# Kernel optimization log

Measured on AMD Instinct MI355X. Metric: run time of the kernel, lower is better.

The kernel has to match this reference:

```python
import jax, jax.numpy as jnp
import numpy as np

B, D = 32768, 256
M, K, V = 1024, 128, 128  # memory_units, key_size, memory_size


def setup_inputs() -> dict:
    key = jax.random.key(0)
    ks = jax.random.split(key, 13)
    g = lambda k, shape, fan: jax.random.normal(k, shape, jnp.float32) * (2.0 / sum(fan)) ** 0.5
    return {
        "x": jax.random.normal(ks[0], (B, D), jnp.float32),
        "Wk": g(ks[1], (D, K), (D, K)), "bk": jnp.zeros((K,), jnp.float32),
        "Wv": g(ks[2], (D, V), (D, V)), "bv": jnp.zeros((V,), jnp.float32),
        "Wq": g(ks[3], (D, K), (D, K)), "bq": jnp.zeros((K,), jnp.float32),
        "Wwr": g(ks[4], (M, M), (M, M)), "bwr": jnp.zeros((M,), jnp.float32),
        "Wrd": g(ks[5], (M, M), (M, M)), "brd": jnp.zeros((M,), jnp.float32),
        "key_memory": g(ks[6], (M, K), (M, K)),
        "value_memory": g(ks[7], (M, V), (M, V)),
    }


def reference(x, Wk, bk, Wv, bv, Wq, bq, Wwr, bwr, Wrd, brd, key_memory, value_memory):
    elu = jax.nn.elu
    key_vec = elu(x @ Wk + bk)      # [B, K]
    val_vec = elu(x @ Wv + bv)      # [B, V]
    qry_vec = elu(x @ Wq + bq)      # [B, K]

    # write attention: Dense(M, softmax) applied to [B, M] scores
    wscores = key_vec @ key_memory.T            # [B, M]
    write_w = jax.nn.softmax(wscores @ Wwr + bwr, axis=-1)  # [B, M]

    inv_b = jnp.float32(1.0 / B)
    # mean over batch of outer products == einsum / B (avoids [B, M, K] intermediate)
    key_mem_new = key_memory + jnp.einsum("bm,bk->mk", write_w, key_vec) * inv_b
    val_mem_new = value_memory + jnp.einsum("bm,bv->mv", write_w, val_vec) * inv_b

    # read uses the UPDATED memories (matches assign_add ordering in call)
    rscores = qry_vec @ key_mem_new.T            # [B, M]
    read_w = jax.nn.softmax(rscores @ Wrd + brd, axis=-1)
    read_vec = read_w @ val_mem_new              # [B, V]
    return read_vec
```

## Files before the change

kernel.cpp:

```cpp
#include <hip/hip_runtime.h>
#include <stdint.h>


typedef short bf16x8 __attribute__((ext_vector_type(8)));
typedef short s16x4  __attribute__((ext_vector_type(4)));
typedef float f32x4  __attribute__((ext_vector_type(4)));

#define MFMA(a, b, c) __builtin_amdgcn_mfma_f32_16x16x32_bf16((a), (b), (c), 0, 0, 0)

__device__ __forceinline__ short f2bf(float f) {
    union { float f; uint32_t u; } v; v.f = f;
    uint32_t r = (v.u + 0x7FFFu + ((v.u >> 16) & 1u)) >> 16;
    return (short)r;
}
__device__ __forceinline__ float bf2f(short h) {
    union { uint32_t u; float f; } v; v.u = ((uint32_t)(uint16_t)h) << 16;
    return v.f;
}
__device__ __forceinline__ uint32_t pack2(float a, float b) {
    return (uint32_t)(uint16_t)f2bf(a) | ((uint32_t)(uint16_t)f2bf(b) << 16);
}
__device__ __forceinline__ unsigned lds_addr(const void* p) {
    return (unsigned)(uintptr_t)(__attribute__((address_space(3))) const void*)p;
}
__device__ __forceinline__ s16x4 trrd(unsigned a) {
    s16x4 d;
    asm volatile("ds_read_b64_tr_b16 %0, %1" : "=v"(d) : "v"(a));
    return d;
}
__device__ __forceinline__ bf16x8 cat8(s16x4 lo, s16x4 hi) {
    bf16x8 r;
    r[0] = lo[0]; r[1] = lo[1]; r[2] = lo[2]; r[3] = lo[3];
    r[4] = hi[0]; r[5] = hi[1]; r[6] = hi[2]; r[7] = hi[3];
    return r;
}
#define GLDS(g, l) __builtin_amdgcn_global_load_lds(                          \
    (const __attribute__((address_space(1))) void*)(g),                       \
    (__attribute__((address_space(3))) void*)(l), 16, 0, 0)

__global__ void kw_kernel(const float* __restrict__ Wk, const float* __restrict__ Wv,
                          const float* __restrict__ Wq, short* __restrict__ wt) {
    const int c = blockIdx.x;
    const int d = threadIdx.x;
    const float* W = (c < 128) ? Wk : ((c < 256) ? Wv : Wq);
    wt[c * 256 + d] = f2bf(W[d * 128 + (c & 127)]);
}

__global__ __launch_bounds__(256) void proj_kernel(
    const float* __restrict__ x, const short* __restrict__ wt,
    const float* __restrict__ bk, const float* __restrict__ bv,
    const float* __restrict__ bq, short* __restrict__ kvq)
{
    const int tid = threadIdx.x;
    const int wave = tid >> 6, lane = tid & 63;
    const int l15 = lane & 15, lq = lane >> 4;
    const int r0 = blockIdx.x * 64;

    f32x4 acc[4][6];
    for (int i = 0; i < 4; ++i)
        for (int j = 0; j < 6; ++j) acc[i][j] = (f32x4){0.f, 0.f, 0.f, 0.f};

    for (int ks = 0; ks < 8; ++ks) {
        const int k0 = ks * 32 + lq * 8;
        bf16x8 a[4];
#pragma unroll
        for (int mf = 0; mf < 4; ++mf) {
            const float* xp = x + (long)(r0 + mf * 16 + l15) * 256 + k0;
            float4 u = *(const float4*)xp;
            float4 v = *(const float4*)(xp + 4);
            bf16x8 t;
            t[0] = f2bf(u.x); t[1] = f2bf(u.y); t[2] = f2bf(u.z); t[3] = f2bf(u.w);
            t[4] = f2bf(v.x); t[5] = f2bf(v.y); t[6] = f2bf(v.z); t[7] = f2bf(v.w);
            a[mf] = t;
        }
#pragma unroll
        for (int nf = 0; nf < 6; ++nf) {
            const int n = wave * 96 + nf * 16 + l15;
            bf16x8 b = *(const bf16x8*)(wt + n * 256 + k0);
#pragma unroll
            for (int mf = 0; mf < 4; ++mf) acc[mf][nf] = MFMA(a[mf], b, acc[mf][nf]);
        }
    }
#pragma unroll
    for (int nf = 0; nf < 6; ++nf) {
        const int col = wave * 96 + nf * 16 + l15;
        const float bias = (col < 128) ? bk[col] : ((col < 256) ? bv[col - 128] : bq[col - 256]);
#pragma unroll
        for (int mf = 0; mf < 4; ++mf) {
#pragma unroll
            for (int rr = 0; rr < 4; ++rr) {
                float v = acc[mf][nf][rr] + bias;
                v = (v > 0.f) ? v : (__expf(v) - 1.f);
                kvq[(long)(r0 + mf * 16 + lq * 4 + rr) * 384 + col] = f2bf(v);
            }
        }
    }
}

template <int COLS>
__global__ __launch_bounds__(256) void pgemm_kernel(
    const void* __restrict__ Agv, const void* __restrict__ Bgv,
    const int lda, const int ldb, const int rchunks, const int rstride,
    float* __restrict__ part)
{
    __shared__ __align__(16) short As[128][72];
    __shared__ __align__(16) short Bs[COLS][72];
    const int tid = threadIdx.x;
    const int wave = tid >> 6, lane = tid & 63;
    const int l15 = lane & 15, lq = lane >> 4;
    const int mt = blockIdx.x, rs = blockIdx.y;
    const long b0 = (long)rs * rstride;
    constexpr int NCF = COLS / 16;
    constexpr int CPT = COLS / 8;

    f32x4 acc[2][NCF];
    for (int s = 0; s < 2; ++s)
        for (int c = 0; c < NCF; ++c) acc[s][c] = (f32x4){0.f, 0.f, 0.f, 0.f};

    const int sr  = (tid & 31) * 2;
    const int am0 = (tid >> 5) * 16;
    const int bc0 = (tid >> 5) * CPT;

    for (int ch = 0; ch < rchunks; ++ch) {
        const long rb = b0 + (long)ch * 64;
        {
            const float* p0 = (const float*)Agv + (rb + sr) * lda + mt * 128 + am0;
            const float* p1 = p0 + lda;
#pragma unroll
            for (int j = 0; j < 16; ++j)
                *(uint32_t*)&As[am0 + j][sr] = pack2(p0[j], p1[j]);
        }
        {
            const float* p0 = (const float*)Bgv + (rb + sr) * ldb + bc0;
            const float* p1 = p0 + ldb;
#pragma unroll
            for (int j = 0; j < CPT; ++j)
                *(uint32_t*)&Bs[bc0 + j][sr] = pack2(p0[j], p1[j]);
        }
        __syncthreads();
#pragma unroll
        for (int ks = 0; ks < 2; ++ks) {
            bf16x8 a0 = *(const bf16x8*)&As[wave * 32 + l15][ks * 32 + lq * 8];
            bf16x8 a1 = *(const bf16x8*)&As[wave * 32 + 16 + l15][ks * 32 + lq * 8];
#pragma unroll
            for (int cf = 0; cf < NCF; ++cf) {
                bf16x8 b = *(const bf16x8*)&Bs[cf * 16 + l15][ks * 32 + lq * 8];
                acc[0][cf] = MFMA(a0, b, acc[0][cf]);
                acc[1][cf] = MFMA(a1, b, acc[1][cf]);
            }
        }
        __syncthreads();
    }
    float* pp = part + (long)rs * 1024 * COLS;
#pragma unroll
    for (int s = 0; s < 2; ++s)
#pragma unroll
        for (int cf = 0; cf < NCF; ++cf)
#pragma unroll
            for (int rr = 0; rr < 4; ++rr) {
                const int m = mt * 128 + wave * 32 + s * 16 + lq * 4 + rr;
                pp[(long)m * COLS + cf * 16 + l15] = acc[s][cf][rr];
            }
}

__global__ void finp_kernel(const float* __restrict__ part, short* __restrict__ pt) {
    const int i = blockIdx.x * 256 + threadIdx.x;
    float s = 0.f;
#pragma unroll
    for (int k = 0; k < 8; ++k) s += part[k * 131072 + i];
    pt[i] = f2bf(s);
}

__global__ __launch_bounds__(256) void eins_kernel(
    const short* __restrict__ w,
    const short* __restrict__ kvq,
    short* __restrict__ part)
{
    __shared__ __align__(16) short As[8192];
    __shared__ __align__(16) short Bs[8192];
    const int tid = threadIdx.x;
    const int wave = tid >> 6, lane = tid & 63;
    const int l15 = lane & 15, lq = lane >> 4;
    const int mt = blockIdx.x >> 1, ct = blockIdx.x & 1;
    const int ks = blockIdx.y;
    const long k0_blk = (long)ks * 1024;

    int aoff[4], boff[4];
    const short* ldsA[4];
    const short* ldsB[4];
#pragma unroll
    for (int q = 0; q < 4; ++q) {
        const int t = wave + q * 4;
        const int s = t * 8 + (lane >> 3);
        const int kl = (s & 15) * 4 + ((lane & 7) >> 1);
        const int m  = (s >> 4) * 16 + (lane & 1) * 8;
        aoff[q] = kl * 1024 + mt * 128 + m;
        boff[q] = kl * 384  + ct * 128 + m;
        ldsA[q] = &As[t * 512];
        ldsB[q] = &Bs[t * 512];
    }

    f32x4 acc[4][4];
    for (int i = 0; i < 4; ++i)
        for (int j = 0; j < 4; ++j) acc[i][j] = (f32x4){0.f, 0.f, 0.f, 0.f};

    const int wr = wave >> 1, wc = wave & 1;
    const unsigned trb  = lds_addr(As) + 2u * (l15 + lq * 64);
    const unsigned trbB = lds_addr(Bs) + 2u * (l15 + lq * 64);

    for (int ch = 0; ch < 16; ++ch) {
        const short* wa = w   + (k0_blk + ch * 64) * 1024;
        const short* kb = kvq + (k0_blk + ch * 64) * 384;
#pragma unroll
        for (int q = 0; q < 4; ++q) {
            GLDS(wa + aoff[q], ldsA[q]);
            GLDS(kb + boff[q], ldsB[q]);
        }
        __syncthreads();
#pragma unroll
        for (int kst = 0; kst < 2; ++kst) {
            s16x4 ah[4][2], bh[4][2];
#pragma unroll
            for (int f = 0; f < 4; ++f) {
#pragma unroll
                for (int h = 0; h < 2; ++h) {
                    ah[f][h] = trrd(trb  + 128u * ((wr * 4 + f) * 16 + kst * 8 + h * 4));
                    bh[f][h] = trrd(trbB + 128u * ((wc * 4 + f) * 16 + kst * 8 + h * 4));
                }
            }
            asm volatile("s_waitcnt lgkmcnt(0)" ::: "memory");
            __builtin_amdgcn_sched_barrier(0);
#pragma unroll
            for (int mf = 0; mf < 4; ++mf) {
                bf16x8 a = cat8(ah[mf][0], ah[mf][1]);
#pragma unroll
                for (int cf = 0; cf < 4; ++cf)
                    acc[mf][cf] = MFMA(a, cat8(bh[cf][0], bh[cf][1]), acc[mf][cf]);
            }
        }
        __syncthreads();
    }

    short* pp = part + ((long)ks * 1024 + mt * 128) * 256 + ct * 128;
#pragma unroll
    for (int mf = 0; mf < 4; ++mf)
#pragma unroll
        for (int cf = 0; cf < 4; ++cf)
#pragma unroll
            for (int rr = 0; rr < 4; ++rr) {
                const int m = wr * 64 + mf * 16 + lq * 4 + rr;
                const int c = wc * 64 + cf * 16 + l15;
                pp[(long)m * 256 + c] = f2bf(acc[mf][cf][rr]);
            }
}

__global__ void finmem_kernel(const short* __restrict__ part,
                              const float* __restrict__ km, const float* __restrict__ vm,
                              float* __restrict__ km_new, short* __restrict__ vmt) {
    const int m = blockIdx.x;
    const int c = threadIdx.x;
    float s = 0.f;
#pragma unroll
    for (int k = 0; k < 32; ++k) s += bf2f(part[k * 262144 + m * 256 + c]);
    s *= (1.0f / 32768.0f);
    if (c < 128) {
        km_new[m * 128 + c] = km[m * 128 + c] + s;
    } else {
        const int v = c - 128;
        vmt[v * 1024 + m] = f2bf(vm[m * 128 + v] + s);
    }
}

__global__ __launch_bounds__(1024, 4) void wexp_kernel(
    const short* __restrict__ kvq, const short* __restrict__ pt,
    const float* __restrict__ bias, short* __restrict__ wout)
{
    __shared__ __align__(16) char kt[16384];
    __shared__ float sred[16][64];
    __shared__ float invs[64];
    const int tid = threadIdx.x;
    const int wave = tid >> 6, lane = tid & 63;
    const int l15 = lane & 15, lq = lane >> 4;
    const int r0 = blockIdx.x * 64;
    const int n0 = wave * 64;

    {
        const int row = tid >> 4;
        const int colb = 16 * ((tid & 15) ^ (row & 7));
        GLDS((const char*)kvq + (long)(r0 + row) * 768 + colb, kt + tid * 16);
    }
    __syncthreads();

    f32x4 acc[4][4];
#pragma unroll
    for (int i = 0; i < 4; ++i)
#pragma unroll
        for (int j = 0; j < 4; ++j) acc[i][j] = (f32x4){0.f, 0.f, 0.f, 0.f};

#pragma unroll
    for (int ks = 0; ks < 4; ++ks) {
        bf16x8 a[4], b[4];
#pragma unroll
        for (int nf = 0; nf < 4; ++nf)
            a[nf] = *(const bf16x8*)(pt + (n0 + nf * 16 + l15) * 128 + ks * 32 + lq * 8);
#pragma unroll
        for (int bf = 0; bf < 4; ++bf) {
            const int r = bf * 16 + l15;
            const int cb = (ks * 64 + lq * 16) ^ ((r & 7) << 4);
            b[bf] = *(const bf16x8*)(kt + r * 256 + cb);
        }
#pragma unroll
        for (int nf = 0; nf < 4; ++nf)
#pragma unroll
            for (int bf = 0; bf < 4; ++bf)
                acc[nf][bf] = MFMA(a[nf], b[bf], acc[nf][bf]);
    }

    float s[4] = {0.f, 0.f, 0.f, 0.f};
#pragma unroll
    for (int nf = 0; nf < 4; ++nf) {
        float4 b4 = *(const float4*)(bias + n0 + nf * 16 + lq * 4);
#pragma unroll
        for (int bf = 0; bf < 4; ++bf) {
            f32x4 t = acc[nf][bf];
            t[0] = __expf(t[0] + b4.x);
            t[1] = __expf(t[1] + b4.y);
            t[2] = __expf(t[2] + b4.z);
            t[3] = __expf(t[3] + b4.w);
            acc[nf][bf] = t;
            s[bf] += (t[0] + t[1]) + (t[2] + t[3]);
        }
    }
#pragma unroll
    for (int bf = 0; bf < 4; ++bf) {
        s[bf] += __shfl_xor(s[bf], 16);
        s[bf] += __shfl_xor(s[bf], 32);
    }
    if (lq == 0) {
#pragma unroll
        for (int bf = 0; bf < 4; ++bf) sred[wave][bf * 16 + l15] = s[bf];
    }
    __syncthreads();
    if (tid < 64) {
        float t = 0.f;
#pragma unroll
        for (int wv = 0; wv < 16; ++wv) t += sred[wv][tid];
        invs[tid] = 1.f / t;
    }
    __syncthreads();

#pragma unroll
    for (int bf = 0; bf < 4; ++bf) {
        const float iv = invs[bf * 16 + l15];
        short* wp = wout + (long)(r0 + bf * 16 + l15) * 1024 + n0 + lq * 4;
#pragma unroll
        for (int nf = 0; nf < 4; ++nf) {
            f32x4 t = acc[nf][bf];
            *(uint2*)(wp + nf * 16) =
                (uint2){pack2(t[0] * iv, t[1] * iv), pack2(t[2] * iv, t[3] * iv)};
        }
    }
}

__global__ __launch_bounds__(1024, 4) void rexp_kernel(
    const short* __restrict__ kvq, const short* __restrict__ pt,
    const float* __restrict__ bias, const short* __restrict__ vmt,
    float* __restrict__ out)
{
    __shared__ __align__(16) char smem[132096];
    __shared__ float sred[16][64];
    __shared__ float invs[64];
    short* Elds = (short*)smem;
    char*  qt   = smem;
    const int tid = threadIdx.x;
    const int wave = tid >> 6, lane = tid & 63;
    const int l15 = lane & 15, lq = lane >> 4;
    const int r0 = blockIdx.x * 64;
    const int n0 = wave * 64;

    {
        const int row = tid >> 4;
        const int colb = 16 * ((tid & 15) ^ (row & 7));
        GLDS((const char*)kvq + (long)(r0 + row) * 768 + 512 + colb, qt + tid * 16);
    }
    __syncthreads();

    f32x4 acc[4][4];
#pragma unroll
    for (int i = 0; i < 4; ++i)
#pragma unroll
        for (int j = 0; j < 4; ++j) acc[i][j] = (f32x4){0.f, 0.f, 0.f, 0.f};

#pragma unroll
    for (int ks = 0; ks < 4; ++ks) {
        bf16x8 a[4], b[4];
#pragma unroll
        for (int nf = 0; nf < 4; ++nf)
            a[nf] = *(const bf16x8*)(pt + (n0 + nf * 16 + l15) * 128 + ks * 32 + lq * 8);
#pragma unroll
        for (int bf = 0; bf < 4; ++bf) {
            const int r = bf * 16 + l15;
            const int cb = (ks * 64 + lq * 16) ^ ((r & 7) << 4);
            b[bf] = *(const bf16x8*)(qt + r * 256 + cb);
        }
#pragma unroll
        for (int nf = 0; nf < 4; ++nf)
#pragma unroll
            for (int bf = 0; bf < 4; ++bf)
                acc[nf][bf] = MFMA(a[nf], b[bf], acc[nf][bf]);
    }

    float s[4] = {0.f, 0.f, 0.f, 0.f};
#pragma unroll
    for (int nf = 0; nf < 4; ++nf) {
        float4 b4 = *(const float4*)(bias + n0 + nf * 16 + lq * 4);
#pragma unroll
        for (int bf = 0; bf < 4; ++bf) {
            f32x4 t = acc[nf][bf];
            t[0] = __expf(t[0] + b4.x);
            t[1] = __expf(t[1] + b4.y);
            t[2] = __expf(t[2] + b4.z);
            t[3] = __expf(t[3] + b4.w);
            acc[nf][bf] = t;
            s[bf] += (t[0] + t[1]) + (t[2] + t[3]);
        }
    }
#pragma unroll
    for (int bf = 0; bf < 4; ++bf) {
        s[bf] += __shfl_xor(s[bf], 16);
        s[bf] += __shfl_xor(s[bf], 32);
    }
    if (lq == 0) {
#pragma unroll
        for (int bf = 0; bf < 4; ++bf) sred[wave][bf * 16 + l15] = s[bf];
    }
    __syncthreads();
    if (tid < 64) {
        float t = 0.f;
#pragma unroll
        for (int wv = 0; wv < 16; ++wv) t += sred[wv][tid];
        invs[tid] = 1.f / t;
    }
    __syncthreads();

#pragma unroll
    for (int bf = 0; bf < 4; ++bf) {
        const float iv = invs[bf * 16 + l15];
        short* ep = Elds + (bf * 16 + l15) * 1032 + n0 + lq * 4;
#pragma unroll
        for (int nf = 0; nf < 4; ++nf) {
            f32x4 t = acc[nf][bf];
            *(uint2*)(ep + nf * 16) =
                (uint2){pack2(t[0] * iv, t[1] * iv), pack2(t[2] * iv, t[3] * iv)};
        }
    }
    __syncthreads();

    const int vf = wave >> 1;
    const int bfp = (wave & 1) * 2;
    f32x4 pv0 = {0.f, 0.f, 0.f, 0.f}, pv1 = {0.f, 0.f, 0.f, 0.f};
    const short* er0 = Elds + (bfp * 16 + l15) * 1032 + lq * 8;
    const short* er1 = er0 + 16 * 1032;
    const short* vp  = vmt + (vf * 16 + l15) * 1024 + lq * 8;
#pragma unroll 8
    for (int ks = 0; ks < 32; ++ks) {
        bf16x8 bv = *(const bf16x8*)(vp + ks * 32);
        pv0 = MFMA(*(const bf16x8*)(er0 + ks * 32), bv, pv0);
        pv1 = MFMA(*(const bf16x8*)(er1 + ks * 32), bv, pv1);
    }
#pragma unroll
    for (int rr = 0; rr < 4; ++rr) {
        out[(long)(r0 + bfp * 16 + lq * 4 + rr) * 128 + vf * 16 + l15] = pv0[rr];
        out[(long)(r0 + (bfp + 1) * 16 + lq * 4 + rr) * 128 + vf * 16 + l15] = pv1[rr];
    }
}

extern "C" void kernel_launch(void* const* d_in, const int* in_sizes, int n_in,
                              void* d_out, int out_size, void* d_ws, size_t ws_size,
                              hipStream_t stream)
{
    const float* x   = (const float*)d_in[0];
    const float* Wk  = (const float*)d_in[1];
    const float* bk  = (const float*)d_in[2];
    const float* Wv  = (const float*)d_in[3];
    const float* bv  = (const float*)d_in[4];
    const float* Wq  = (const float*)d_in[5];
    const float* bq  = (const float*)d_in[6];
    const float* Wwr = (const float*)d_in[7];
    const float* bwr = (const float*)d_in[8];
    const float* Wrd = (const float*)d_in[9];
    const float* brd = (const float*)d_in[10];
    const float* km  = (const float*)d_in[11];
    const float* vm  = (const float*)d_in[12];
    float* out = (float*)d_out;

    char* ws = (char*)d_ws;
    short* kvq  = (short*)(ws + 0);
    short* w    = (short*)(ws + 25165824);
    float* part = (float*)(ws + 92274688);
    short* p1t  = (short*)(ws + 109051904);
    short* p2t  = (short*)(ws + 109314048);
    float* kmn  = (float*)(ws + 109576192);
    short* vmt  = (short*)(ws + 110100480);
    short* wt   = (short*)(ws + 110362624);
    if (ws_size < 110559232u) return;

    kw_kernel<<<384, 256, 0, stream>>>(Wk, Wv, Wq, wt);
    proj_kernel<<<512, 256, 0, stream>>>(x, wt, bk, bv, bq, kvq);
    pgemm_kernel<128><<<dim3(8, 8), 256, 0, stream>>>(Wwr, km, 1024, 128, 2, 128, part);
    finp_kernel<<<512, 256, 0, stream>>>(part, p1t);
    wexp_kernel<<<512, 1024, 0, stream>>>(kvq, p1t, bwr, w);
    eins_kernel<<<dim3(16, 32), 256, 0, stream>>>(w, kvq, (short*)part);
    finmem_kernel<<<1024, 256, 0, stream>>>((const short*)part, km, vm, kmn, vmt);
    pgemm_kernel<128><<<dim3(8, 8), 256, 0, stream>>>(Wrd, kmn, 1024, 128, 2, 128, part);
    finp_kernel<<<512, 256, 0, stream>>>(part, p2t);
    rexp_kernel<<<512, 1024, 0, stream>>>(kvq, p2t, brd, vmt, out);
}
```

Measured before the change: 203.9 us.

## Replace read softmax kernel with flash-attention style fused streaming kernel

The final read stage no longer materialises the full 64x1024 softmax row tile in LDS. Each wave now owns 16 rows and streams 64-column tiles of the score projection and value memory through small LDS buffers. It computes exp scores, packs them to bf16 and feeds them directly into a 16x16x16 MFMA against value memory, normalising once at the end. This cuts LDS footprint and block size (256 threads instead of 1024) and drops the block-wide reduction syncs, at the cost of per-tile barriers and global reloads of pt/vmt for every block.

```diff
diff --git a/kernel.cpp b/kernel.cpp
--- a/kernel.cpp
+++ b/kernel.cpp
@@ -7,6 +7,11 @@
 typedef float f32x4  __attribute__((ext_vector_type(4)));
 
 #define MFMA(a, b, c) __builtin_amdgcn_mfma_f32_16x16x32_bf16((a), (b), (c), 0, 0, 0)
+
+__device__ __forceinline__ f32x4 MFMA16(s16x4 a, s16x4 b, f32x4 c) {
+    asm("v_mfma_f32_16x16x16_bf16 %0, %1, %2, %0" : "+v"(c) : "v"(a), "v"(b));
+    return c;
+}
 
 __device__ __forceinline__ short f2bf(float f) {
     union { float f; uint32_t u; } v; v.f = f;
@@ -362,116 +367,109 @@
     }
 }
 
-__global__ __launch_bounds__(1024, 4) void rexp_kernel(
+__global__ __launch_bounds__(256, 4) void fatt_kernel(
     const short* __restrict__ kvq, const short* __restrict__ pt,
     const float* __restrict__ bias, const short* __restrict__ vmt,
     float* __restrict__ out)
 {
-    __shared__ __align__(16) char smem[132096];
-    __shared__ float sred[16][64];
-    __shared__ float invs[64];
-    short* Elds = (short*)smem;
-    char*  qt   = smem;
+    __shared__ __align__(16) char ptl[16384];
+    __shared__ __align__(16) char vtl[16384];
     const int tid = threadIdx.x;
     const int wave = tid >> 6, lane = tid & 63;
     const int l15 = lane & 15, lq = lane >> 4;
-    const int r0 = blockIdx.x * 64;
-    const int n0 = wave * 64;
-
-    {
-        const int row = tid >> 4;
-        const int colb = 16 * ((tid & 15) ^ (row & 7));
-        GLDS((const char*)kvq + (long)(r0 + row) * 768 + 512 + colb, qt + tid * 16);
-    }
-    __syncthreads();
-
-    f32x4 acc[4][4];
-#pragma unroll
-    for (int i = 0; i < 4; ++i)
-#pragma unroll
-        for (int j = 0; j < 4; ++j) acc[i][j] = (f32x4){0.f, 0.f, 0.f, 0.f};
-
-#pragma unroll
-    for (int ks = 0; ks < 4; ++ks) {
-        bf16x8 a[4], b[4];
-#pragma unroll
-        for (int nf = 0; nf < 4; ++nf)
-            a[nf] = *(const bf16x8*)(pt + (n0 + nf * 16 + l15) * 128 + ks * 32 + lq * 8);
-#pragma unroll
-        for (int bf = 0; bf < 4; ++bf) {
-            const int r = bf * 16 + l15;
-            const int cb = (ks * 64 + lq * 16) ^ ((r & 7) << 4);
-            b[bf] = *(const bf16x8*)(qt + r * 256 + cb);
-        }
-#pragma unroll
-        for (int nf = 0; nf < 4; ++nf)
-#pragma unroll
-            for (int bf = 0; bf < 4; ++bf)
-                acc[nf][bf] = MFMA(a[nf], b[bf], acc[nf][bf]);
-    }
-
-    float s[4] = {0.f, 0.f, 0.f, 0.f};
-#pragma unroll
-    for (int nf = 0; nf < 4; ++nf) {
-        float4 b4 = *(const float4*)(bias + n0 + nf * 16 + lq * 4);
-#pragma unroll
-        for (int bf = 0; bf < 4; ++bf) {
-            f32x4 t = acc[nf][bf];
+    const int r0 = blockIdx.x * 64 + wave * 16;
+
+    bf16x8 qf[4];
+#pragma unroll
+    for (int ks = 0; ks < 4; ++ks)
+        qf[ks] = *(const bf16x8*)(kvq + (long)(r0 + l15) * 384 + 256 + ks * 32 + lq * 8);
+
+    f32x4 o[8];
+#pragma unroll
+    for (int i = 0; i < 8; ++i) o[i] = (f32x4){0.f, 0.f, 0.f, 0.f};
+    float s = 0.f;
+
+    const char* ptb = (const char*)pt;
+    const char* vmb = (const char*)vmt;
+
+    int pn[4], pin[4], vv[4], vin[4];
+    char* pdst[4];
+    char* vdst[4];
+#pragma unroll
+    for (int c = 0; c < 4; ++c) {
+        const int L = tid * 16 + c * 4096;
+        pn[c] = L >> 8; pin[c] = L & 255;
+        vv[c] = L >> 7; vin[c] = L & 127;
+        pdst[c] = ptl + pn[c] * 256 + (pin[c] ^ ((pn[c] & 7) << 4));
+        vdst[c] = vtl + vv[c] * 128 + (vin[c] ^ ((vv[c] & 7) << 4));
+    }
+
+    for (int nt = 0; nt < 16; ++nt) {
+        const int n0 = nt * 64;
+        uint4 pg[4], vg[4];
+#pragma unroll
+        for (int c = 0; c < 4; ++c) {
+            pg[c] = *(const uint4*)(ptb + (long)(n0 + pn[c]) * 256 + pin[c]);
+            vg[c] = *(const uint4*)(vmb + (long)vv[c] * 2048 + n0 * 2 + vin[c]);
+        }
+        __syncthreads();
+#pragma unroll
+        for (int c = 0; c < 4; ++c) {
+            *(uint4*)pdst[c] = pg[c];
+            *(uint4*)vdst[c] = vg[c];
+        }
+        __syncthreads();
+
+        f32x4 acc[4];
+#pragma unroll
+        for (int nf = 0; nf < 4; ++nf) acc[nf] = (f32x4){0.f, 0.f, 0.f, 0.f};
+#pragma unroll
+        for (int ks = 0; ks < 4; ++ks) {
+#pragma unroll
+            for (int nf = 0; nf < 4; ++nf) {
+                const int n = nf * 16 + l15;
+                bf16x8 a = *(const bf16x8*)(ptl + n * 256 +
+                                            ((ks * 64 + lq * 16) ^ ((n & 7) << 4)));
+                acc[nf] = MFMA(a, qf[ks], acc[nf]);
+            }
+        }
+
+        s16x4 e[4];
+#pragma unroll
+        for (int nf = 0; nf < 4; ++nf) {
+            float4 b4 = *(const float4*)(bias + n0 + nf * 16 + lq * 4);
+            f32x4 t = acc[nf];
             t[0] = __expf(t[0] + b4.x);
             t[1] = __expf(t[1] + b4.y);
             t[2] = __expf(t[2] + b4.z);
             t[3] = __expf(t[3] + b4.w);
-            acc[nf][bf] = t;
-            s[bf] += (t[0] + t[1]) + (t[2] + t[3]);
-        }
-    }
-#pragma unroll
-    for (int bf = 0; bf < 4; ++bf) {
-        s[bf] += __shfl_xor(s[bf], 16);
-        s[bf] += __shfl_xor(s[bf], 32);
-    }
-    if (lq == 0) {
-#pragma unroll
-        for (int bf = 0; bf < 4; ++bf) sred[wave][bf * 16 + l15] = s[bf];
-    }
-    __syncthreads();
-    if (tid < 64) {
-        float t = 0.f;
-#pragma unroll
-        for (int wv = 0; wv < 16; ++wv) t += sred[wv][tid];
-        invs[tid] = 1.f / t;
-    }
-    __syncthreads();
-
-#pragma unroll
-    for (int bf = 0; bf < 4; ++bf) {
-        const float iv = invs[bf * 16 + l15];
-        short* ep = Elds + (bf * 16 + l15) * 1032 + n0 + lq * 4;
+            s += (t[0] + t[1]) + (t[2] + t[3]);
+            union { uint2 u; s16x4 q; } pk;
+            pk.u = (uint2){pack2(t[0], t[1]), pack2(t[2], t[3])};
+            e[nf] = pk.q;
+        }
+
 #pragma unroll
         for (int nf = 0; nf < 4; ++nf) {
-            f32x4 t = acc[nf][bf];
-            *(uint2*)(ep + nf * 16) =
-                (uint2){pack2(t[0] * iv, t[1] * iv), pack2(t[2] * iv, t[3] * iv)};
-        }
-    }
-    __syncthreads();
-
-    const int vf = wave >> 1;
-    const int bfp = (wave & 1) * 2;
-    f32x4 pv0 = {0.f, 0.f, 0.f, 0.f}, pv1 = {0.f, 0.f, 0.f, 0.f};
-    const short* er0 = Elds + (bfp * 16 + l15) * 1032 + lq * 8;
-    const short* er1 = er0 + 16 * 1032;
-    const short* vp  = vmt + (vf * 16 + l15) * 1024 + lq * 8;
-#pragma unroll 8
-    for (int ks = 0; ks < 32; ++ks) {
-        bf16x8 bv = *(const bf16x8*)(vp + ks * 32);
-        pv0 = MFMA(*(const bf16x8*)(er0 + ks * 32), bv, pv0);
-        pv1 = MFMA(*(const bf16x8*)(er1 + ks * 32), bv, pv1);
-    }
-#pragma unroll
-    for (int rr = 0; rr < 4; ++rr) {
-        out[(long)(r0 + bfp * 16 + lq * 4 + rr) * 128 + vf * 16 + l15] = pv0[rr];
-        out[(long)(r0 + (bfp + 1) * 16 + lq * 4 + rr) * 128 + vf * 16 + l15] = pv1[rr];
+#pragma unroll
+            for (int vt = 0; vt < 8; ++vt) {
+                const int v = vt * 16 + l15;
+                s16x4 av = *(const s16x4*)(vtl + v * 128 +
+                                           ((nf * 32 + lq * 8) ^ ((v & 7) << 4)));
+                o[vt] = MFMA16(av, e[nf], o[vt]);
+            }
+        }
+    }
+
+    s += __shfl_xor(s, 16);
+    s += __shfl_xor(s, 32);
+    const float inv = 1.f / s;
+    float* op = out + (long)(r0 + l15) * 128 + lq * 4;
+#pragma unroll
+    for (int vt = 0; vt < 8; ++vt) {
+        f32x4 t = o[vt];
+        t[0] *= inv; t[1] *= inv; t[2] *= inv; t[3] *= inv;
+        *(f32x4*)(op + vt * 16) = t;
     }
 }
 
@@ -514,5 +512,5 @@
     finmem_kernel<<<1024, 256, 0, stream>>>((const short*)part, km, vm, kmn, vmt);
     pgemm_kernel<128><<<dim3(8, 8), 256, 0, stream>>>(Wrd, kmn, 1024, 128, 2, 128, part);
     finp_kernel<<<512, 256, 0, stream>>>(part, p2t);
-    rexp_kernel<<<512, 1024, 0, stream>>>(kvq, p2t, brd, vmt, out);
-}
+    fatt_kernel<<<512, 256, 0, stream>>>(kvq, p2t, brd, vmt, out);
+}
```

New measurement: 254.9 us. +25.0%, slower.
